# Kernel tuning notes

Measured on AMD Instinct MI355X. Metric: run time of the kernel, lower is better.

The kernel has to match this reference:

```python
import jax, jax.numpy as jnp
import numpy as np

HEADS = 8


def setup_inputs() -> dict:
    key = jax.random.key(0)
    ks = jax.random.split(key, 6)
    b, n, dim = 8, 4096, 512
    s = 0.02
    return {
        "x": jax.random.normal(ks[0], (b, n, dim), jnp.float32),
        "Wq": jax.random.normal(ks[1], (dim, dim), jnp.float32) * s,
        "Wk": jax.random.normal(ks[2], (dim, dim), jnp.float32) * s,
        "Wv": jax.random.normal(ks[3], (dim, dim), jnp.float32) * s,
        "Wo": jax.random.normal(ks[4], (dim, dim), jnp.float32) * s,
        "bo": jnp.zeros((dim,), jnp.float32),
    }


def reference(x, Wq, Wk, Wv, Wo, bo):
    b, n, dim = x.shape
    heads = HEADS
    d = dim // heads
    g = int(np.sqrt(n))  # square grid, n chosen as perfect square (no padding)
    scale = d ** -0.5

    def proj(W):
        # [b, n, dim] -> [b, heads, g, g, d]
        t = jnp.einsum('bne,ef->bnf', x, W)
        return t.reshape(b, g, g, heads, d).transpose(0, 3, 1, 2, 4)

    q, k, v = proj(Wq), proj(Wk), proj(Wv)

    # row-wise attention: attend along last grid axis for each row i
    dots_row = jnp.einsum('bnijd,bnikd->bnijk', q, k) * scale
    out_row = jnp.einsum('bnijk,bnikd->bnijd', jax.nn.softmax(dots_row, axis=-1), v)

    # column-wise attention (as in source: transpose grid axes, same einsum pattern)
    q_c, k_c, v_c = (t.swapaxes(2, 3) for t in (q, k, v))
    dots_col = jnp.einsum('bnjid,bnkid->bnjik', q_c, k_c) * scale
    out_col = jnp.einsum('bnjik,bnkid->bnjid', jax.nn.softmax(dots_col, axis=-1), v_c)

    out = out_row + out_col.swapaxes(2, 3)  # [b, heads, g, g, d]
    out = out.transpose(0, 2, 3, 1, 4).reshape(b, n, dim)
    return jnp.einsum('bne,ef->bnf', out, Wo) + bo
```

## Files before the change

kernel.cpp:

```cpp
#include <hip/hip_runtime.h>
#include <hip/hip_bf16.h>
#include <stdint.h>


typedef __bf16 bf16_t;
typedef __bf16 bf16x4v __attribute__((ext_vector_type(4)));
typedef __bf16 bf16x8 __attribute__((ext_vector_type(8)));
typedef float  f32x4  __attribute__((ext_vector_type(4)));

#define GLD16(gp, lp)                                                                  \
  __builtin_amdgcn_global_load_lds((__attribute__((address_space(1))) const void*)(gp),\
                                   (__attribute__((address_space(3))) void*)(lp),      \
                                   16, 0, 0)

__device__ __forceinline__ float  bf2f(bf16_t x) { return (float)x; }
__device__ __forceinline__ bf16_t f2bf(float x)  { return (bf16_t)x; }

__global__ __launch_bounds__(256) void cvt_x(const float* __restrict__ X,
                                             bf16_t* __restrict__ Y, int n4)
{
  int i = blockIdx.x * blockDim.x + threadIdx.x;
  if (i < n4) {
    float4 v = ((const float4*)X)[i];
    bf16x4v o;
    o[0] = f2bf(v.x); o[1] = f2bf(v.y); o[2] = f2bf(v.z); o[3] = f2bf(v.w);
    ((bf16x4v*)Y)[i] = o;
  }
}

__global__ void wt_kernel(const float* __restrict__ Wq, const float* __restrict__ Wk,
                          const float* __restrict__ Wv, const float* __restrict__ Wo,
                          bf16_t* __restrict__ WT)
{
  __shared__ bf16_t tile[32][33];
  const int mat = blockIdx.z;
  const float* W = (mat == 0) ? Wq : (mat == 1) ? Wk : (mat == 2) ? Wv : Wo;
  bf16_t* dst = WT + (size_t)mat * 262144;
  const int tx = threadIdx.x, ty = threadIdx.y;
  const int x0 = blockIdx.x * 32, y0 = blockIdx.y * 32;
#pragma unroll
  for (int i = 0; i < 32; i += 8)
    tile[ty + i][tx] = f2bf(W[(size_t)(y0 + ty + i) * 512 + x0 + tx]);
  __syncthreads();
#pragma unroll
  for (int i = 0; i < 32; i += 8)
    dst[(size_t)(x0 + ty + i) * 512 + y0 + tx] = tile[tx][ty + i];
}

template <bool STORE_F32>
__global__ __launch_bounds__(256) void gemm_bt(
    const bf16_t* __restrict__ A,
    const bf16_t* __restrict__ BT,
    void* __restrict__ Cp,
    const float* __restrict__ bias,
    int Nd)
{
  constexpr int Kd = 512;
  __shared__ __align__(16) bf16_t smem[16384];
  bf16_t* const As[2] = { smem,        smem + 8192  };
  bf16_t* const Bs[2] = { smem + 4096, smem + 12288 };

  const int tid  = threadIdx.x;
  const int lane = tid & 63, w = tid >> 6;
  const int quad = lane >> 4, r16 = lane & 15;
  const int m0 = blockIdx.y * 128, n0 = blockIdx.x * 128;
  const int wm = (w & 1) * 64, wn = (w >> 1) * 64;

  f32x4 acc[4][4] = {};

  const int srow = w * 32 + (lane >> 2);
  const int scol = (lane & 3) * 8;
  const bf16_t* Ag = A  + (size_t)(m0 + srow) * Kd + scol;
  const bf16_t* Bg = BT + (size_t)(n0 + srow) * Kd + scol;

  for (int k0 = 0; k0 < Kd; k0 += 64) {
    __syncthreads();
    GLD16(Ag + k0,                As[0] + w * 1024);
    GLD16(Ag + k0 + 16 * Kd,      As[0] + w * 1024 + 512);
    GLD16(Bg + k0,                Bs[0] + w * 1024);
    GLD16(Bg + k0 + 16 * Kd,      Bs[0] + w * 1024 + 512);
    GLD16(Ag + k0 + 32,           As[1] + w * 1024);
    GLD16(Ag + k0 + 32 + 16 * Kd, As[1] + w * 1024 + 512);
    GLD16(Bg + k0 + 32,           Bs[1] + w * 1024);
    GLD16(Bg + k0 + 32 + 16 * Kd, Bs[1] + w * 1024 + 512);
    __builtin_amdgcn_s_waitcnt(0x0f70);
    __syncthreads();

#pragma unroll
    for (int ps = 0; ps < 2; ++ps) {
      bf16x8 af[4], bfr[4];
#pragma unroll
      for (int i = 0; i < 4; ++i)
        af[i] = *(const bf16x8*)&As[ps][(wm + i * 16 + r16) * 32 + quad * 8];
#pragma unroll
      for (int j = 0; j < 4; ++j)
        bfr[j] = *(const bf16x8*)&Bs[ps][(wn + j * 16 + r16) * 32 + quad * 8];
#pragma unroll
      for (int i = 0; i < 4; ++i)
#pragma unroll
        for (int j = 0; j < 4; ++j)
          acc[i][j] = __builtin_amdgcn_mfma_f32_16x16x32_bf16(af[i], bfr[j], acc[i][j], 0, 0, 0);
    }
  }

  if (STORE_F32) {
#pragma unroll
    for (int i = 0; i < 4; ++i) {
#pragma unroll
      for (int j = 0; j < 4; ++j) {
        const int row = m0 + wm + i * 16 + quad * 4;
        const int col = n0 + wn + j * 16 + r16;
        const float bv = bias ? bias[col] : 0.0f;
#pragma unroll
        for (int rg = 0; rg < 4; ++rg)
          ((float*)Cp)[(size_t)(row + rg) * Nd + col] = acc[i][j][rg] + bv;
      }
    }
  } else {
    bf16_t* Es = smem;
#pragma unroll
    for (int p = 0; p < 2; ++p) {
      __syncthreads();
      if ((w & 1) == p) {
#pragma unroll
        for (int i = 0; i < 4; ++i)
#pragma unroll
          for (int j = 0; j < 4; ++j)
#pragma unroll
            for (int rg = 0; rg < 4; ++rg)
              Es[(i * 16 + quad * 4 + rg) * 132 + wn + j * 16 + r16] = f2bf(acc[i][j][rg]);
      }
      __syncthreads();
#pragma unroll
      for (int rd = 0; rd < 4; ++rd) {
        const int row = rd * 16 + (tid >> 4);
        const int col = (tid & 15) * 8;
        *(bf16x8*)&((bf16_t*)Cp)[(size_t)(m0 + p * 64 + row) * Nd + n0 + col] =
            *(const bf16x8*)&Es[row * 132 + col];
      }
    }
  }
}

__global__ __launch_bounds__(256) void cc_attn(
    const bf16_t* __restrict__ QKV, bf16_t* __restrict__ Aout)
{
  __shared__ __align__(16) bf16_t Qs[64 * 72];
  __shared__ __align__(16) bf16_t Ks[64 * 72];
  __shared__ __align__(16) bf16_t VsT[64 * 70];

  const int gidx = blockIdx.x;
  const int r = gidx & 63, h = (gidx >> 6) & 7, b = gidx >> 9;
  const int tid = threadIdx.x, lane = tid & 63, w = tid >> 6;
  const int quad = lane >> 4, r16 = lane & 15;
  const size_t row0 = (size_t)b * 4096 + (size_t)r * 64;

  {
    const int row = tid >> 2, seg = tid & 3;
    const bf16_t* gp = QKV + (row0 + row) * 1536 + h * 64 + seg * 16;
    *(bf16x8*)&Qs[row * 72 + seg * 16]     = *(const bf16x8*)&gp[0];
    *(bf16x8*)&Qs[row * 72 + seg * 16 + 8] = *(const bf16x8*)&gp[8];
    *(bf16x8*)&Ks[row * 72 + seg * 16]     = *(const bf16x8*)&gp[512];
    *(bf16x8*)&Ks[row * 72 + seg * 16 + 8] = *(const bf16x8*)&gp[520];
    bf16x8 v0 = *(const bf16x8*)&gp[1024];
    bf16x8 v1 = *(const bf16x8*)&gp[1032];
#pragma unroll
    for (int e = 0; e < 8; ++e) {
      VsT[(seg * 16 + e) * 70 + row]     = v0[e];
      VsT[(seg * 16 + 8 + e) * 70 + row] = v1[e];
    }
  }
  __syncthreads();

  f32x4 sacc[4] = {};
#pragma unroll
  for (int ks = 0; ks < 2; ++ks) {
    bf16x8 aq = *(const bf16x8*)&Qs[(w * 16 + r16) * 72 + ks * 32 + quad * 8];
#pragma unroll
    for (int nj = 0; nj < 4; ++nj) {
      bf16x8 bk = *(const bf16x8*)&Ks[(nj * 16 + r16) * 72 + ks * 32 + quad * 8];
      sacc[nj] = __builtin_amdgcn_mfma_f32_16x16x32_bf16(aq, bk, sacc[nj], 0, 0, 0);
    }
  }

  float ex[4][4];
  float mx[4], sm[4];
#pragma unroll
  for (int rg = 0; rg < 4; ++rg) {
    float m = -3.0e38f;
#pragma unroll
    for (int nj = 0; nj < 4; ++nj) {
      ex[nj][rg] = sacc[nj][rg] * 0.125f;
      m = fmaxf(m, ex[nj][rg]);
    }
    m = fmaxf(m, __shfl_xor(m, 1));
    m = fmaxf(m, __shfl_xor(m, 2));
    m = fmaxf(m, __shfl_xor(m, 4));
    m = fmaxf(m, __shfl_xor(m, 8));
    mx[rg] = m;
    float s = 0.f;
#pragma unroll
    for (int nj = 0; nj < 4; ++nj) { ex[nj][rg] = __expf(ex[nj][rg] - m); s += ex[nj][rg]; }
    s += __shfl_xor(s, 1);
    s += __shfl_xor(s, 2);
    s += __shfl_xor(s, 4);
    s += __shfl_xor(s, 8);
    sm[rg] = 2.0f / s;
  }

  __syncthreads();
#pragma unroll
  for (int nj = 0; nj < 4; ++nj)
#pragma unroll
    for (int rg = 0; rg < 4; ++rg)
      Qs[(w * 16 + quad * 4 + rg) * 72 + nj * 16 + r16] = f2bf(ex[nj][rg] * sm[rg]);
  __syncthreads();

  f32x4 oacc[4] = {};
#pragma unroll
  for (int ks = 0; ks < 2; ++ks) {
    bf16x8 ap = *(const bf16x8*)&Qs[(w * 16 + r16) * 72 + ks * 32 + quad * 8];
#pragma unroll
    for (int nj = 0; nj < 4; ++nj) {
      bf16x8 bv = *(const bf16x8*)&VsT[(nj * 16 + r16) * 70 + ks * 32 + quad * 8];
      oacc[nj] = __builtin_amdgcn_mfma_f32_16x16x32_bf16(ap, bv, oacc[nj], 0, 0, 0);
    }
  }

  {
    bf16_t* Es = Ks;
#pragma unroll
    for (int nj = 0; nj < 4; ++nj)
#pragma unroll
      for (int rg = 0; rg < 4; ++rg)
        Es[(w * 16 + quad * 4 + rg) * 72 + nj * 16 + r16] = f2bf(oacc[nj][rg]);
    __syncthreads();
    const size_t obase = row0 * 512 + (size_t)h * 64;
#pragma unroll
    for (int rd = 0; rd < 2; ++rd) {
      const int row = rd * 32 + (tid >> 3);
      const int col = (tid & 7) * 8;
      *(bf16x8*)&Aout[obase + (size_t)row * 512 + col] = *(const bf16x8*)&Es[row * 72 + col];
    }
  }
}

extern "C" void kernel_launch(void* const* d_in, const int* in_sizes, int n_in,
                              void* d_out, int out_size, void* d_ws, size_t ws_size,
                              hipStream_t stream)
{
  const float* x  = (const float*)d_in[0];
  const float* Wq = (const float*)d_in[1];
  const float* Wk = (const float*)d_in[2];
  const float* Wv = (const float*)d_in[3];
  const float* Wo = (const float*)d_in[4];
  const float* bo = (const float*)d_in[5];

  bf16_t* ws = (bf16_t*)d_ws;
  bf16_t* WT  = ws;
  bf16_t* xbf = ws + 1048576;
  bf16_t* QKV = xbf + 16777216;
  bf16_t* Ab  = xbf;

  cvt_x<<<dim3(16384), 256, 0, stream>>>(x, xbf, 4194304);
  wt_kernel<<<dim3(16, 16, 4), dim3(32, 8), 0, stream>>>(Wq, Wk, Wv, Wo, WT);

  gemm_bt<false><<<dim3(12, 256), 256, 0, stream>>>(xbf, WT, QKV, nullptr, 1536);

  cc_attn<<<dim3(4096), 256, 0, stream>>>(QKV, Ab);

  gemm_bt<true><<<dim3(4, 256), 256, 0, stream>>>(Ab, WT + 786432, d_out, bo, 512);
}
```

Before: 262.9 us.

## Widen QKV GEMM tile to 128x256 and add XCD-aware block remapping

Templates the GEMM on the N tile width and launches the QKV projection with 128x256 tiles, halving the grid and reusing each A tile across twice as many output columns. Adds a block-index remap that assigns contiguous M row-blocks to each XCD so that blocks sharing an A tile land on the same L2. The wider tile doubles the accumulator registers and LDS for B, which may reduce occupancy. Also removes an unused max array in the attention softmax.

```diff
diff --git a/kernel.cpp b/kernel.cpp
--- a/kernel.cpp
+++ b/kernel.cpp
@@ -47,7 +47,7 @@
     dst[(size_t)(x0 + ty + i) * 512 + y0 + tx] = tile[tx][ty + i];
 }
 
-template <bool STORE_F32>
+template <bool STORE_F32, int BN>
 __global__ __launch_bounds__(256) void gemm_bt(
     const bf16_t* __restrict__ A,
     const bf16_t* __restrict__ BT,
@@ -56,50 +56,60 @@
     int Nd)
 {
   constexpr int Kd = 512;
-  __shared__ __align__(16) bf16_t smem[16384];
-  bf16_t* const As[2] = { smem,        smem + 8192  };
-  bf16_t* const Bs[2] = { smem + 4096, smem + 12288 };
+  constexpr int JT = BN / 32;
+  constexpr int RBW = BN / 4;
+  __shared__ __align__(16) bf16_t smem[8192 + 2 * BN * 32];
+  bf16_t* const As[2] = { smem,        smem + 4096 };
+  bf16_t* const Bs[2] = { smem + 8192, smem + 8192 + BN * 32 };
 
   const int tid  = threadIdx.x;
   const int lane = tid & 63, w = tid >> 6;
   const int quad = lane >> 4, r16 = lane & 15;
-  const int m0 = blockIdx.y * 128, n0 = blockIdx.x * 128;
-  const int wm = (w & 1) * 64, wn = (w >> 1) * 64;
-
-  f32x4 acc[4][4] = {};
-
-  const int srow = w * 32 + (lane >> 2);
-  const int scol = (lane & 3) * 8;
-  const bf16_t* Ag = A  + (size_t)(m0 + srow) * Kd + scol;
-  const bf16_t* Bg = BT + (size_t)(n0 + srow) * Kd + scol;
+
+  const int G = gridDim.x;
+  const int l = blockIdx.y * G + blockIdx.x;
+  const int xcd = l & 7, slot = l >> 3;
+  const int mb = xcd * (gridDim.y >> 3) + slot / G;
+  const int nb = slot % G;
+  const int m0 = mb * 128, n0 = nb * BN;
+
+  const int wm = (w & 1) * 64, wn = (w >> 1) * (BN / 2);
+
+  f32x4 acc[4][JT] = {};
+
+  const int rA = w * 32  + (lane >> 2);
+  const int rB = w * RBW + (lane >> 2);
+  const int sc = (lane & 3) * 8;
+  const bf16_t* Ag = A  + (size_t)(m0 + rA) * Kd + sc;
+  const bf16_t* Bg = BT + (size_t)(n0 + rB) * Kd + sc;
 
   for (int k0 = 0; k0 < Kd; k0 += 64) {
     __syncthreads();
-    GLD16(Ag + k0,                As[0] + w * 1024);
-    GLD16(Ag + k0 + 16 * Kd,      As[0] + w * 1024 + 512);
-    GLD16(Bg + k0,                Bs[0] + w * 1024);
-    GLD16(Bg + k0 + 16 * Kd,      Bs[0] + w * 1024 + 512);
-    GLD16(Ag + k0 + 32,           As[1] + w * 1024);
-    GLD16(Ag + k0 + 32 + 16 * Kd, As[1] + w * 1024 + 512);
-    GLD16(Bg + k0 + 32,           Bs[1] + w * 1024);
-    GLD16(Bg + k0 + 32 + 16 * Kd, Bs[1] + w * 1024 + 512);
+#pragma unroll
+    for (int ps = 0; ps < 2; ++ps) {
+      const int kp = k0 + ps * 32;
+      GLD16(Ag + kp,           As[ps] + w * 1024);
+      GLD16(Ag + kp + 16 * Kd, As[ps] + w * 1024 + 512);
+#pragma unroll
+      for (int rr = 0; rr < BN / 64; ++rr)
+        GLD16(Bg + kp + rr * 16 * Kd, Bs[ps] + w * RBW * 32 + rr * 512);
+    }
     __builtin_amdgcn_s_waitcnt(0x0f70);
     __syncthreads();
 
 #pragma unroll
     for (int ps = 0; ps < 2; ++ps) {
-      bf16x8 af[4], bfr[4];
+      bf16x8 af[4];
 #pragma unroll
       for (int i = 0; i < 4; ++i)
         af[i] = *(const bf16x8*)&As[ps][(wm + i * 16 + r16) * 32 + quad * 8];
 #pragma unroll
-      for (int j = 0; j < 4; ++j)
-        bfr[j] = *(const bf16x8*)&Bs[ps][(wn + j * 16 + r16) * 32 + quad * 8];
-#pragma unroll
-      for (int i = 0; i < 4; ++i)
-#pragma unroll
-        for (int j = 0; j < 4; ++j)
-          acc[i][j] = __builtin_amdgcn_mfma_f32_16x16x32_bf16(af[i], bfr[j], acc[i][j], 0, 0, 0);
+      for (int j = 0; j < JT; ++j) {
+        bf16x8 bfr = *(const bf16x8*)&Bs[ps][(wn + j * 16 + r16) * 32 + quad * 8];
+#pragma unroll
+        for (int i = 0; i < 4; ++i)
+          acc[i][j] = __builtin_amdgcn_mfma_f32_16x16x32_bf16(af[i], bfr, acc[i][j], 0, 0, 0);
+      }
     }
   }
 
@@ -107,7 +117,7 @@
 #pragma unroll
     for (int i = 0; i < 4; ++i) {
 #pragma unroll
-      for (int j = 0; j < 4; ++j) {
+      for (int j = 0; j < JT; ++j) {
         const int row = m0 + wm + i * 16 + quad * 4;
         const int col = n0 + wn + j * 16 + r16;
         const float bv = bias ? bias[col] : 0.0f;
@@ -117,6 +127,7 @@
       }
     }
   } else {
+    constexpr int PITCH = BN + 8;
     bf16_t* Es = smem;
 #pragma unroll
     for (int p = 0; p < 2; ++p) {
@@ -125,18 +136,20 @@
 #pragma unroll
         for (int i = 0; i < 4; ++i)
 #pragma unroll
-          for (int j = 0; j < 4; ++j)
+          for (int j = 0; j < JT; ++j)
 #pragma unroll
             for (int rg = 0; rg < 4; ++rg)
-              Es[(i * 16 + quad * 4 + rg) * 132 + wn + j * 16 + r16] = f2bf(acc[i][j][rg]);
+              Es[(i * 16 + quad * 4 + rg) * PITCH + wn + j * 16 + r16] = f2bf(acc[i][j][rg]);
       }
       __syncthreads();
-#pragma unroll
-      for (int rd = 0; rd < 4; ++rd) {
-        const int row = rd * 16 + (tid >> 4);
-        const int col = (tid & 15) * 8;
+      constexpr int TPR = BN / 8;
+      constexpr int RPI = 256 / TPR;
+#pragma unroll
+      for (int rd = 0; rd < 64 / RPI; ++rd) {
+        const int row = rd * RPI + tid / TPR;
+        const int col = (tid % TPR) * 8;
         *(bf16x8*)&((bf16_t*)Cp)[(size_t)(m0 + p * 64 + row) * Nd + n0 + col] =
-            *(const bf16x8*)&Es[row * 132 + col];
+            *(const bf16x8*)&Es[row * PITCH + col];
       }
     }
   }
@@ -184,7 +197,7 @@
   }
 
   float ex[4][4];
-  float mx[4], sm[4];
+  float sm[4];
 #pragma unroll
   for (int rg = 0; rg < 4; ++rg) {
     float m = -3.0e38f;
@@ -197,7 +210,6 @@
     m = fmaxf(m, __shfl_xor(m, 2));
     m = fmaxf(m, __shfl_xor(m, 4));
     m = fmaxf(m, __shfl_xor(m, 8));
-    mx[rg] = m;
     float s = 0.f;
 #pragma unroll
     for (int nj = 0; nj < 4; ++nj) { ex[nj][rg] = __expf(ex[nj][rg] - m); s += ex[nj][rg]; }
@@ -265,9 +277,9 @@
   cvt_x<<<dim3(16384), 256, 0, stream>>>(x, xbf, 4194304);
   wt_kernel<<<dim3(16, 16, 4), dim3(32, 8), 0, stream>>>(Wq, Wk, Wv, Wo, WT);
 
-  gemm_bt<false><<<dim3(12, 256), 256, 0, stream>>>(xbf, WT, QKV, nullptr, 1536);
+  gemm_bt<false, 256><<<dim3(6, 256), 256, 0, stream>>>(xbf, WT, QKV, nullptr, 1536);
 
   cc_attn<<<dim3(4096), 256, 0, stream>>>(QKV, Ab);
 
-  gemm_bt<true><<<dim3(4, 256), 256, 0, stream>>>(Ab, WT + 786432, d_out, bo, 512);
-}
+  gemm_bt<true, 128><<<dim3(4, 256), 256, 0, stream>>>(Ab, WT + 786432, d_out, bo, 512);
+}
```

Result: slower. 299.5 us (+13.9%).
